# Kernel optimization log

Hardware: AMD Instinct MI355X
Metric: run time of the kernel (lower is better)

The kernel has to match this reference:

```python
import jax, jax.numpy as jnp
import numpy as np
import math

B, S, D, K = 8, 2048, 1024, 64
EPS = 1e-5

def _ln(x):
    m = jnp.mean(x, axis=-1, keepdims=True)
    v = jnp.mean((x - m) ** 2, axis=-1, keepdims=True)
    return (x - m) * jax.lax.rsqrt(v + EPS)

def setup_inputs() -> dict:
    key = jax.random.key(0)
    ks = jax.random.split(key, 14)
    s = 0.02
    return {
        "x":  jax.random.normal(ks[0], (B, S, D), dtype=jnp.float32),
        "Wk": jax.random.normal(ks[1], (D, K), dtype=jnp.float32) * s,
        "bk": jnp.zeros((K,), dtype=jnp.float32),
        "Wq": jax.random.normal(ks[2], (D, K), dtype=jnp.float32) * s,
        "bq": jnp.zeros((K,), dtype=jnp.float32),
        "Wv": jax.random.normal(ks[3], (D, D), dtype=jnp.float32) * s,
        "bv": jnp.zeros((D,), dtype=jnp.float32),
        "Wb": jax.random.normal(ks[4], (D, 1), dtype=jnp.float32) * s,
        "bb": jnp.zeros((1,), dtype=jnp.float32),
        "W1": jax.random.normal(ks[5], (D, D), dtype=jnp.float32) * s,
        "b1": jnp.zeros((D,), dtype=jnp.float32),
        "g1": jnp.ones((D,), dtype=jnp.float32),
        "be1": jnp.zeros((D,), dtype=jnp.float32),
    }

def reference(x, Wk, bk, Wq, bq, Wv, bv, Wb, bb, W1, b1, g1, be1):
    scale = 1.0 / math.sqrt(K)
    keys    = (jnp.einsum('bsd,dk->bsk', x, Wk) + bk) * scale   # [B,S,K]
    queries = jnp.einsum('bsd,dk->bsk', x, Wq) + bq             # [B,S,K]
    values  = jnp.einsum('bsd,de->bse', x, Wv) + bv             # [B,S,D]
    biases  = jnp.einsum('bsd,do->bso', x, Wb) + bb             # [B,S,1]
    # scores[b,i,j] = keys[b,i] . queries[b,j] + biases[b,i]
    scores = jax.nn.sigmoid(jnp.einsum('bik,bjk->bij', keys, queries) + biases)
    attention = jnp.einsum('bij,bjd->bid', scores, values)      # [B,S,D]
    res = _ln(x + attention) * g1 + be1
    feedforward = jax.nn.relu(jnp.einsum('bsd,de->bse', res, W1) + b1)
    return _ln(res + feedforward)
```

## Files before the change

kernel.cpp:

```cpp
#include <hip/hip_runtime.h>
#include <math.h>


typedef __bf16 bf16_t;
typedef __bf16 bf16x2_t __attribute__((ext_vector_type(2)));
typedef __bf16 bf16x4_t __attribute__((ext_vector_type(4)));
typedef __bf16 bf16x8_t __attribute__((ext_vector_type(8)));
typedef float  f32x4    __attribute__((ext_vector_type(4)));

#define DEV static __device__ __forceinline__

DEV void gll16(const void* g, void* l) {
  __builtin_amdgcn_global_load_lds(
      (const __attribute__((address_space(1))) void*)g,
      (__attribute__((address_space(3))) void*)l, 16, 0, 0);
}

template <int MODE, int MFAST>
__global__ __launch_bounds__(512, 2) void gemm256(
    const bf16_t* __restrict__ A, const bf16_t* __restrict__ B,
    bf16_t* __restrict__ C, int K, int lda, int ldb, int ldc,
    long sAb, long sBb, long sCb, const float* __restrict__ aux0) {
  const int gx = gridDim.x, gy = gridDim.y;
  const int gxy = gx * gy;
  const int nwg = gxy * (int)gridDim.z;
  const int orig = blockIdx.x + gx * blockIdx.y + gxy * blockIdx.z;
  const int lid = (orig & 7) * (nwg >> 3) + (orig >> 3);
  const int bz = lid / gxy;
  const int rem = lid - bz * gxy;
  const int bx = MFAST ? (rem / gy) : (rem % gx);
  const int by = MFAST ? (rem % gy) : (rem / gx);

  A += (long)bz * sAb;
  B += (long)bz * sBb;
  const int m0 = by * 256, n0 = bx * 256;

  __shared__ bf16_t As[2][2][256 * 32];
  __shared__ bf16_t Bs[2][2][256 * 32];

  const int tid = threadIdx.x;
  const int wid = tid >> 6, l = tid & 63;
  const int wr = wid >> 2, wc = wid & 3;
  const int lr = l & 15, lh = l >> 4;

  const int sRow = tid >> 2;
  const int sSl = (tid & 3) ^ ((tid >> 3) & 3);
  const bf16_t* Asrc = A + (long)(m0 + sRow) * lda + sSl * 8;
  const bf16_t* Bsrc = B + (long)(n0 + sRow) * ldb + sSl * 8;
  const long aStep = (long)128 * lda, bStep = (long)128 * ldb;

#define STAGE_A(b, h, kt) do { \
    const bf16_t* s_ = Asrc + (kt) * 64 + (h) * 32; \
    gll16(s_,         &As[b][h][tid * 8]); \
    gll16(s_ + aStep, &As[b][h][4096 + tid * 8]); } while (0)
#define STAGE_B(b, h, kt) do { \
    const bf16_t* s_ = Bsrc + (kt) * 64 + (h) * 32; \
    gll16(s_,         &Bs[b][h][tid * 8]); \
    gll16(s_ + bStep, &Bs[b][h][4096 + tid * 8]); } while (0)

  const int sw = (lh ^ ((lr >> 1) & 3)) * 8;
  const int aOff = (wr * 128 + lr) * 32 + sw;
  const int bOff = (wc * 64 + lr) * 32 + sw;

  f32x4 acc[8][4] = {};
  const int NT = K >> 6;

  STAGE_A(0, 0, 0); STAGE_B(0, 0, 0); STAGE_A(0, 1, 0); STAGE_B(0, 1, 0);
  asm volatile("s_waitcnt vmcnt(4)" ::: "memory");
  __builtin_amdgcn_s_barrier();

#define PHASE_SYNC() do { \
    __builtin_amdgcn_sched_barrier(0); \
    __builtin_amdgcn_s_barrier(); \
    asm volatile("s_waitcnt lgkmcnt(0)" ::: "memory"); \
    __builtin_amdgcn_sched_barrier(0); } while (0)
#define MFMA_LO() do { \
    __builtin_amdgcn_s_setprio(1); \
    _Pragma("unroll") for (int m = 0; m < 4; ++m) \
    _Pragma("unroll") for (int n = 0; n < 4; ++n) \
      acc[m][n] = __builtin_amdgcn_mfma_f32_16x16x32_bf16(aF[m], bF[n], acc[m][n], 0, 0, 0); \
    __builtin_amdgcn_s_setprio(0); } while (0)
#define MFMA_HI() do { \
    __builtin_amdgcn_s_setprio(1); \
    _Pragma("unroll") for (int m = 0; m < 4; ++m) \
    _Pragma("unroll") for (int n = 0; n < 4; ++n) \
      acc[m + 4][n] = __builtin_amdgcn_mfma_f32_16x16x32_bf16(aG[m], bF[n], acc[m + 4][n], 0, 0, 0); \
    __builtin_amdgcn_s_setprio(0); } while (0)

  for (int t = 0; t < NT; ++t) {
    const int p = t & 1, q = p ^ 1;
    const bool pf = (t + 1 < NT);
    bf16x8_t bF[4], aF[4], aG[4];

#pragma unroll
    for (int n = 0; n < 4; ++n) bF[n] = *(const bf16x8_t*)&Bs[p][0][bOff + n * 512];
#pragma unroll
    for (int m = 0; m < 4; ++m) aF[m] = *(const bf16x8_t*)&As[p][0][aOff + m * 512];
    if (pf) STAGE_A(q, 0, t + 1);
    PHASE_SYNC();
    MFMA_LO();

#pragma unroll
    for (int m = 0; m < 4; ++m) aG[m] = *(const bf16x8_t*)&As[p][0][aOff + (m + 4) * 512];
    if (pf) {
      STAGE_B(q, 0, t + 1);
      asm volatile("s_waitcnt vmcnt(4)" ::: "memory");
    } else {
      asm volatile("s_waitcnt vmcnt(0)" ::: "memory");
    }
    PHASE_SYNC();
    MFMA_HI();

#pragma unroll
    for (int n = 0; n < 4; ++n) bF[n] = *(const bf16x8_t*)&Bs[p][1][bOff + n * 512];
#pragma unroll
    for (int m = 0; m < 4; ++m) aF[m] = *(const bf16x8_t*)&As[p][1][aOff + m * 512];
    if (pf) STAGE_A(q, 1, t + 1);
    PHASE_SYNC();
    MFMA_LO();

#pragma unroll
    for (int m = 0; m < 4; ++m) aG[m] = *(const bf16x8_t*)&As[p][1][aOff + (m + 4) * 512];
    if (pf) {
      STAGE_B(q, 1, t + 1);
      asm volatile("s_waitcnt vmcnt(4)" ::: "memory");
    }
    PHASE_SYNC();
    MFMA_HI();
  }
#undef STAGE_A
#undef STAGE_B
#undef PHASE_SYNC
#undef MFMA_LO
#undef MFMA_HI

  bf16_t* Cb = C + (long)bz * sCb;
  const int rowb = m0 + wr * 128 + lh * 4;
  const int colb = n0 + wc * 64 + lr;
#pragma unroll
  for (int m = 0; m < 8; ++m)
#pragma unroll
    for (int n = 0; n < 4; ++n) {
      const f32x4 v = acc[m][n];
      const int cc = colb + n * 16;
#pragma unroll
      for (int r = 0; r < 4; ++r) {
        const int rr = rowb + m * 16 + r;
        const float val = v[r];
        if constexpr (MODE == 1) {
          Cb[(long)rr * ldc + cc] = (bf16_t)(val + aux0[rr]);
        } else if constexpr (MODE == 3) {
          Cb[(long)rr * ldc + cc] = (bf16_t)val;
        } else {
          Cb[(long)rr * ldc + cc] = (bf16_t)fmaxf(val + aux0[cc], 0.0f);
        }
      }
    }
}

template <int MODE, int MFAST>
__global__ __launch_bounds__(256) void gemm_bt(
    const bf16_t* __restrict__ A, const bf16_t* __restrict__ B,
    void* __restrict__ Cv, int M, int N, int K, int lda, int ldb, int ldc,
    long sAb, long sBb, long sCb,
    const float* __restrict__ aux0, const float* __restrict__ aux1, long sAux) {
  const int gx = gridDim.x, gy = gridDim.y;
  const int gxy = gx * gy;
  const int nwg = gxy * (int)gridDim.z;
  const int orig = blockIdx.x + gx * blockIdx.y + gxy * blockIdx.z;
  const int q = nwg >> 3, r8 = nwg & 7;
  const int xcd = orig & 7, seq = orig >> 3;
  const int lid = (xcd < r8 ? xcd * (q + 1) : r8 * (q + 1) + (xcd - r8) * q) + seq;
  const int bz = lid / gxy;
  const int rem = lid - bz * gxy;
  const int bx = MFAST ? (rem / gy) : (rem % gx);
  const int by = MFAST ? (rem % gy) : (rem / gx);

  A += (long)bz * sAb;
  B += (long)bz * sBb;
  const float* a0 = (MODE == 2) ? (aux0 + (long)bz * sAux) : aux0;

  const int m0 = by * 128;
  const int n0 = bx * 128;

  __shared__ bf16_t As[2][128 * 32];
  __shared__ bf16_t Bs[2][128 * 32];

  const int tid = threadIdx.x;
  const int w = tid >> 6, l = tid & 63;
  const int wr = w >> 1, wc = w & 1;
  const int lr = l & 15, lh = l >> 4;

  const int srow = l >> 2;
  const int scol = (((l & 3) ^ (srow & 3)) << 3);

  f32x4 acc[4][4] = {};

  auto stage = [&](int buf, int k0) {
#pragma unroll
    for (int half = 0; half < 2; ++half) {
      const int i = 2 * w + half;
      const int row = (i << 4) + srow;
      gll16(A + (long)(m0 + row) * lda + k0 + scol, &As[buf][i << 9]);
      gll16(B + (long)(n0 + row) * ldb + k0 + scol, &Bs[buf][i << 9]);
    }
  };

  stage(0, 0);
  __syncthreads();
  int cur = 0;
  const int sw = ((lh ^ (lr & 3)) << 3);

  for (int k0 = 0; k0 < K; k0 += 32) {
    if (k0 + 32 < K) stage(cur ^ 1, k0 + 32);

    bf16x8_t af[4], bfm[4];
#pragma unroll
    for (int m = 0; m < 4; ++m)
      af[m] = *(const bf16x8_t*)(&As[cur][(((wr << 6) + (m << 4) + lr) << 5) + sw]);
#pragma unroll
    for (int n = 0; n < 4; ++n)
      bfm[n] = *(const bf16x8_t*)(&Bs[cur][(((wc << 6) + (n << 4) + lr) << 5) + sw]);
#pragma unroll
    for (int m = 0; m < 4; ++m)
#pragma unroll
      for (int n = 0; n < 4; ++n)
        acc[m][n] = __builtin_amdgcn_mfma_f32_16x16x32_bf16(af[m], bfm[n], acc[m][n], 0, 0, 0);

    __syncthreads();
    cur ^= 1;
  }

  const int rowbase = m0 + (wr << 6) + (lh << 2);
  const int colbase = n0 + (wc << 6) + lr;
#pragma unroll
  for (int m = 0; m < 4; ++m) {
#pragma unroll
    for (int n = 0; n < 4; ++n) {
      const f32x4 v = acc[m][n];
      const int cc = colbase + (n << 4);
#pragma unroll
      for (int r = 0; r < 4; ++r) {
        const int rr = rowbase + (m << 4) + r;
        const float val = v[r];
        if constexpr (MODE == 0) {
          const float b = (cc < 64) ? aux0[cc] : aux1[cc - 64];
          const float s = (cc < 64) ? 0.125f : 1.0f;
          ((bf16_t*)Cv)[(long)rr * ldc + cc] = (bf16_t)((val + b) * s);
        } else {
          const float zz = val + a0[rr];
          const float e = __expf(-zz);
          const float sg = __builtin_amdgcn_rcpf(1.0f + e);
          ((bf16_t*)Cv)[(long)bz * sCb + (long)rr * ldc + cc] = (bf16_t)sg;
        }
      }
    }
  }
}

__global__ __launch_bounds__(256) void cast_bf16_kernel(
    const float* __restrict__ in, bf16_t* __restrict__ out, long n) {
  long i = ((long)blockIdx.x * 256 + threadIdx.x) * 4;
  const long step = (long)gridDim.x * 1024;
  for (; i < n; i += step) {
    const float4 v = *(const float4*)(in + i);
    bf16x4_t o;
    o[0] = (bf16_t)v.x; o[1] = (bf16_t)v.y; o[2] = (bf16_t)v.z; o[3] = (bf16_t)v.w;
    *(bf16x4_t*)(out + i) = o;
  }
}

__global__ __launch_bounds__(256) void transpose_cast_kernel(
    const float* __restrict__ in, bf16_t* __restrict__ out, int R, int C) {
  __shared__ float t[32][33];
  const int c0 = blockIdx.x * 32, r0 = blockIdx.y * 32;
  const int tx = threadIdx.x & 31, ty = threadIdx.x >> 5;
#pragma unroll
  for (int i = 0; i < 4; ++i) {
    const int rl = ty * 4 + i;
    t[rl][tx] = in[(long)(r0 + rl) * C + c0 + tx];
  }
  __syncthreads();
#pragma unroll
  for (int i = 0; i < 4; ++i) {
    const int rl = ty * 4 + i;
    out[(long)(c0 + rl) * R + r0 + tx] = (bf16_t)t[tx][rl];
  }
}

__global__ __launch_bounds__(256) void bias_kernel(
    const bf16_t* __restrict__ x, const float* __restrict__ Wb,
    const float* __restrict__ bb, float* __restrict__ biases) {
  const int r = blockIdx.x * 4 + (threadIdx.x >> 6);
  const int l = threadIdx.x & 63;
  const bf16_t* xr = x + (long)r * 1024;
  float s = 0.f;
#pragma unroll
  for (int i = 0; i < 8; ++i) {
    const bf16x2_t v = *(const bf16x2_t*)(xr + (l << 1) + (i << 7));
    const float2 wv = *(const float2*)(Wb + (l << 1) + (i << 7));
    s += (float)v[0] * wv.x + (float)v[1] * wv.y;
  }
#pragma unroll
  for (int off = 1; off < 64; off <<= 1) s += __shfl_xor(s, off);
  if (l == 0) biases[r] = s + bb[0];
}

DEV float2 block_sum2(float s, float ss) {
#pragma unroll
  for (int off = 1; off < 64; off <<= 1) {
    s += __shfl_xor(s, off);
    ss += __shfl_xor(ss, off);
  }
  __shared__ float bs[4], bss[4];
  const int w = threadIdx.x >> 6, l = threadIdx.x & 63;
  if (l == 0) { bs[w] = s; bss[w] = ss; }
  __syncthreads();
  s = bs[0] + bs[1] + bs[2] + bs[3];
  ss = bss[0] + bss[1] + bss[2] + bss[3];
  return make_float2(s, ss);
}

__global__ __launch_bounds__(256) void ln1_kernel(
    const bf16_t* __restrict__ x, const bf16_t* __restrict__ attn,
    const float* __restrict__ g, const float* __restrict__ be,
    bf16_t* __restrict__ res) {
  const long r = blockIdx.x;
  const int t = threadIdx.x;
  const bf16x4_t xv = *(const bf16x4_t*)(x + r * 1024 + t * 4);
  const bf16x4_t av = *(const bf16x4_t*)(attn + r * 1024 + t * 4);
  const float y0 = (float)xv[0] + (float)av[0], y1 = (float)xv[1] + (float)av[1];
  const float y2 = (float)xv[2] + (float)av[2], y3 = (float)xv[3] + (float)av[3];
  const float2 s2 = block_sum2(y0 + y1 + y2 + y3, y0 * y0 + y1 * y1 + y2 * y2 + y3 * y3);
  const float mean = s2.x * (1.0f / 1024.0f);
  const float var = s2.y * (1.0f / 1024.0f) - mean * mean;
  const float rs = rsqrtf(var + 1e-5f);
  const int c = t * 4;
  bf16x4_t o;
  o[0] = (bf16_t)((y0 - mean) * rs * g[c + 0] + be[c + 0]);
  o[1] = (bf16_t)((y1 - mean) * rs * g[c + 1] + be[c + 1]);
  o[2] = (bf16_t)((y2 - mean) * rs * g[c + 2] + be[c + 2]);
  o[3] = (bf16_t)((y3 - mean) * rs * g[c + 3] + be[c + 3]);
  *(bf16x4_t*)(res + r * 1024 + c) = o;
}

__global__ __launch_bounds__(256) void ln2_kernel(
    const bf16_t* __restrict__ res, const bf16_t* __restrict__ h,
    float* __restrict__ out) {
  const long r = blockIdx.x;
  const int t = threadIdx.x;
  const bf16x4_t rv = *(const bf16x4_t*)(res + r * 1024 + t * 4);
  const bf16x4_t hv = *(const bf16x4_t*)(h + r * 1024 + t * 4);
  const float y0 = (float)rv[0] + (float)hv[0], y1 = (float)rv[1] + (float)hv[1];
  const float y2 = (float)rv[2] + (float)hv[2], y3 = (float)rv[3] + (float)hv[3];
  const float2 s2 = block_sum2(y0 + y1 + y2 + y3, y0 * y0 + y1 * y1 + y2 * y2 + y3 * y3);
  const float mean = s2.x * (1.0f / 1024.0f);
  const float var = s2.y * (1.0f / 1024.0f) - mean * mean;
  const float rs = rsqrtf(var + 1e-5f);
  float4 o;
  o.x = (y0 - mean) * rs; o.y = (y1 - mean) * rs;
  o.z = (y2 - mean) * rs; o.w = (y3 - mean) * rs;
  ((float4*)(out + r * 1024))[t] = o;
}

extern "C" void kernel_launch(void* const* d_in, const int* in_sizes, int n_in,
                              void* d_out, int out_size, void* d_ws, size_t ws_size,
                              hipStream_t stream) {
  const float* x   = (const float*)d_in[0];
  const float* Wk  = (const float*)d_in[1];
  const float* bk  = (const float*)d_in[2];
  const float* Wq  = (const float*)d_in[3];
  const float* bq  = (const float*)d_in[4];
  const float* Wv  = (const float*)d_in[5];
  const float* bv  = (const float*)d_in[6];
  const float* Wb  = (const float*)d_in[7];
  const float* bb  = (const float*)d_in[8];
  const float* W1  = (const float*)d_in[9];
  const float* b1  = (const float*)d_in[10];
  const float* g1  = (const float*)d_in[11];
  const float* be1 = (const float*)d_in[12];
  float* out = (float*)d_out;

  char* ws = (char*)d_ws;
  bf16_t* x_bf    = (bf16_t*)(ws + 0);
  bf16_t* vt_bf   = (bf16_t*)(ws + 33554432);
  bf16_t* kq_bf   = (bf16_t*)(ws + 67108864);
  bf16_t* Wkqt    = (bf16_t*)(ws + 71303168);
  bf16_t* Wvt     = (bf16_t*)(ws + 71565312);
  bf16_t* W1t     = (bf16_t*)(ws + 73662464);
  float*  biases  = (float*) (ws + 75759616);
  bf16_t* scores  = (bf16_t*)(ws + 75825152);
  bf16_t* attn_bf = (bf16_t*)(ws + 142934016);
  bf16_t* res_bf  = (bf16_t*)(ws + 176488448);
  bf16_t* h_bf    = attn_bf;

  const long BS = 16384;

  cast_bf16_kernel<<<8192, 256, 0, stream>>>(x, x_bf, BS * 1024);
  transpose_cast_kernel<<<dim3(2, 32), 256, 0, stream>>>(Wk, Wkqt, 1024, 64);
  transpose_cast_kernel<<<dim3(2, 32), 256, 0, stream>>>(Wq, Wkqt + 64 * 1024, 1024, 64);
  transpose_cast_kernel<<<dim3(32, 32), 256, 0, stream>>>(Wv, Wvt, 1024, 1024);
  transpose_cast_kernel<<<dim3(32, 32), 256, 0, stream>>>(W1, W1t, 1024, 1024);
  bias_kernel<<<4096, 256, 0, stream>>>(x_bf, Wb, bb, biases);

  gemm_bt<0, 0><<<dim3(1, 128, 1), 256, 0, stream>>>(
      x_bf, Wkqt, kq_bf, 16384, 128, 1024, 1024, 1024, 128, 0, 0, 0, bk, bq, 0);

  gemm256<1, 1><<<dim3(64, 4, 1), 512, 0, stream>>>(
      Wvt, x_bf, vt_bf, 1024, 1024, 1024, 16384, 0, 0, 0, bv);

  gemm_bt<2, 0><<<dim3(16, 16, 8), 256, 0, stream>>>(
      kq_bf, kq_bf + 64, scores, 2048, 2048, 64, 128, 128, 2048,
      2048L * 128, 2048L * 128, 2048L * 2048, biases, nullptr, 2048);

  gemm256<3, 0><<<dim3(4, 8, 8), 512, 0, stream>>>(
      scores, vt_bf, attn_bf, 2048, 2048, 16384, 1024,
      2048L * 2048, 2048, 2048L * 1024, nullptr);

  ln1_kernel<<<16384, 256, 0, stream>>>(x_bf, attn_bf, g1, be1, res_bf);

  gemm256<4, 0><<<dim3(4, 64, 1), 512, 0, stream>>>(
      res_bf, W1t, h_bf, 1024, 1024, 1024, 1024, 0, 0, 0, b1);

  ln2_kernel<<<16384, 256, 0, stream>>>(res_bf, h_bf, out);
}
```

Before: 254.4 us.

## Stage GEMM epilogues through LDS for vector stores; fuse cast with bias

Both GEMM kernels now write their outputs through a swizzled shared-memory tile (reusing the staging buffers as one flat array) and then emit 16-byte coalesced global stores, instead of scattered 2-byte stores per accumulator element. The input cast and the bias dot product are fused into one kernel that reads x in fp32 once. This removes a launch and an extra pass over x_bf, and bias now uses fp32 x rather than bf16-rounded x. The vmcnt wait in the last phase is made unconditional, and the epilogue adds barriers and LDS traffic.

```diff
diff --git a/kernel.cpp b/kernel.cpp
--- a/kernel.cpp
+++ b/kernel.cpp
@@ -3,7 +3,6 @@
 
 
 typedef __bf16 bf16_t;
-typedef __bf16 bf16x2_t __attribute__((ext_vector_type(2)));
 typedef __bf16 bf16x4_t __attribute__((ext_vector_type(4)));
 typedef __bf16 bf16x8_t __attribute__((ext_vector_type(8)));
 typedef float  f32x4    __attribute__((ext_vector_type(4)));
@@ -35,8 +34,9 @@
   B += (long)bz * sBb;
   const int m0 = by * 256, n0 = bx * 256;
 
-  __shared__ bf16_t As[2][2][256 * 32];
-  __shared__ bf16_t Bs[2][2][256 * 32];
+  __shared__ bf16_t SM[65536];
+#define ASH(b, h) (&SM[(((b)*2 + (h)) << 13)])
+#define BSH(b, h) (&SM[32768 + (((b)*2 + (h)) << 13)])
 
   const int tid = threadIdx.x;
   const int wid = tid >> 6, l = tid & 63;
@@ -51,12 +51,12 @@
 
 #define STAGE_A(b, h, kt) do { \
     const bf16_t* s_ = Asrc + (kt) * 64 + (h) * 32; \
-    gll16(s_,         &As[b][h][tid * 8]); \
-    gll16(s_ + aStep, &As[b][h][4096 + tid * 8]); } while (0)
+    gll16(s_,         ASH(b, h) + tid * 8); \
+    gll16(s_ + aStep, ASH(b, h) + 4096 + tid * 8); } while (0)
 #define STAGE_B(b, h, kt) do { \
     const bf16_t* s_ = Bsrc + (kt) * 64 + (h) * 32; \
-    gll16(s_,         &Bs[b][h][tid * 8]); \
-    gll16(s_ + bStep, &Bs[b][h][4096 + tid * 8]); } while (0)
+    gll16(s_,         BSH(b, h) + tid * 8); \
+    gll16(s_ + bStep, BSH(b, h) + 4096 + tid * 8); } while (0)
 
   const int sw = (lh ^ ((lr >> 1) & 3)) * 8;
   const int aOff = (wr * 128 + lr) * 32 + sw;
@@ -93,15 +93,15 @@
     bf16x8_t bF[4], aF[4], aG[4];
 
 #pragma unroll
-    for (int n = 0; n < 4; ++n) bF[n] = *(const bf16x8_t*)&Bs[p][0][bOff + n * 512];
-#pragma unroll
-    for (int m = 0; m < 4; ++m) aF[m] = *(const bf16x8_t*)&As[p][0][aOff + m * 512];
+    for (int n = 0; n < 4; ++n) bF[n] = *(const bf16x8_t*)(BSH(p, 0) + bOff + n * 512);
+#pragma unroll
+    for (int m = 0; m < 4; ++m) aF[m] = *(const bf16x8_t*)(ASH(p, 0) + aOff + m * 512);
     if (pf) STAGE_A(q, 0, t + 1);
     PHASE_SYNC();
     MFMA_LO();
 
 #pragma unroll
-    for (int m = 0; m < 4; ++m) aG[m] = *(const bf16x8_t*)&As[p][0][aOff + (m + 4) * 512];
+    for (int m = 0; m < 4; ++m) aG[m] = *(const bf16x8_t*)(ASH(p, 0) + aOff + (m + 4) * 512);
     if (pf) {
       STAGE_B(q, 0, t + 1);
       asm volatile("s_waitcnt vmcnt(4)" ::: "memory");
@@ -112,19 +112,17 @@
     MFMA_HI();
 
 #pragma unroll
-    for (int n = 0; n < 4; ++n) bF[n] = *(const bf16x8_t*)&Bs[p][1][bOff + n * 512];
-#pragma unroll
-    for (int m = 0; m < 4; ++m) aF[m] = *(const bf16x8_t*)&As[p][1][aOff + m * 512];
+    for (int n = 0; n < 4; ++n) bF[n] = *(const bf16x8_t*)(BSH(p, 1) + bOff + n * 512);
+#pragma unroll
+    for (int m = 0; m < 4; ++m) aF[m] = *(const bf16x8_t*)(ASH(p, 1) + aOff + m * 512);
     if (pf) STAGE_A(q, 1, t + 1);
     PHASE_SYNC();
     MFMA_LO();
 
 #pragma unroll
-    for (int m = 0; m < 4; ++m) aG[m] = *(const bf16x8_t*)&As[p][1][aOff + (m + 4) * 512];
-    if (pf) {
-      STAGE_B(q, 1, t + 1);
-      asm volatile("s_waitcnt vmcnt(4)" ::: "memory");
-    }
+    for (int m = 0; m < 4; ++m) aG[m] = *(const bf16x8_t*)(ASH(p, 1) + aOff + (m + 4) * 512);
+    if (pf) STAGE_B(q, 1, t + 1);
+    asm volatile("s_waitcnt vmcnt(4)" ::: "memory");
     PHASE_SYNC();
     MFMA_HI();
   }
@@ -134,28 +132,38 @@
 #undef MFMA_LO
 #undef MFMA_HI
 
-  bf16_t* Cb = C + (long)bz * sCb;
-  const int rowb = m0 + wr * 128 + lh * 4;
-  const int colb = n0 + wc * 64 + lr;
-#pragma unroll
-  for (int m = 0; m < 8; ++m)
-#pragma unroll
-    for (int n = 0; n < 4; ++n) {
-      const f32x4 v = acc[m][n];
-      const int cc = colb + n * 16;
-#pragma unroll
-      for (int r = 0; r < 4; ++r) {
-        const int rr = rowb + m * 16 + r;
-        const float val = v[r];
-        if constexpr (MODE == 1) {
-          Cb[(long)rr * ldc + cc] = (bf16_t)(val + aux0[rr]);
-        } else if constexpr (MODE == 3) {
-          Cb[(long)rr * ldc + cc] = (bf16_t)val;
-        } else {
-          Cb[(long)rr * ldc + cc] = (bf16_t)fmaxf(val + aux0[cc], 0.0f);
+  __builtin_amdgcn_s_barrier();
+  {
+    const int rowb = wr * 128 + lh * 4;
+    const int colb = wc * 64 + lr;
+#pragma unroll
+    for (int m = 0; m < 8; ++m)
+#pragma unroll
+      for (int n = 0; n < 4; ++n) {
+        const f32x4 v = acc[m][n];
+        const int cl = colb + n * 16;
+#pragma unroll
+        for (int r = 0; r < 4; ++r) {
+          const int rl = rowb + m * 16 + r;
+          float val = v[r];
+          if constexpr (MODE == 1) val += aux0[m0 + rl];
+          else if constexpr (MODE == 4) val = fmaxf(val + aux0[n0 + cl], 0.0f);
+          SM[rl * 256 + (cl ^ (lh << 4))] = (bf16_t)val;
         }
       }
+    __builtin_amdgcn_s_barrier();
+    bf16_t* Cb = C + (long)bz * sCb;
+    const int chunk = tid & 31, rsub = tid >> 5;
+#pragma unroll
+    for (int pp = 0; pp < 16; ++pp) {
+      const int rl = pp * 16 + rsub;
+      const int sc = chunk ^ (((rl >> 2) & 3) << 1);
+      const bf16x8_t vv = *(const bf16x8_t*)&SM[rl * 256 + sc * 8];
+      *(bf16x8_t*)&Cb[(long)(m0 + rl) * ldc + n0 + chunk * 8] = vv;
     }
+  }
+#undef ASH
+#undef BSH
 }
 
 template <int MODE, int MFAST>
@@ -183,8 +191,9 @@
   const int m0 = by * 128;
   const int n0 = bx * 128;
 
-  __shared__ bf16_t As[2][128 * 32];
-  __shared__ bf16_t Bs[2][128 * 32];
+  __shared__ bf16_t SM[16384];
+#define ASH(b) (&SM[(b) << 12])
+#define BSH(b) (&SM[8192 + ((b) << 12)])
 
   const int tid = threadIdx.x;
   const int w = tid >> 6, l = tid & 63;
@@ -201,8 +210,8 @@
     for (int half = 0; half < 2; ++half) {
       const int i = 2 * w + half;
       const int row = (i << 4) + srow;
-      gll16(A + (long)(m0 + row) * lda + k0 + scol, &As[buf][i << 9]);
-      gll16(B + (long)(n0 + row) * ldb + k0 + scol, &Bs[buf][i << 9]);
+      gll16(A + (long)(m0 + row) * lda + k0 + scol, ASH(buf) + (i << 9));
+      gll16(B + (long)(n0 + row) * ldb + k0 + scol, BSH(buf) + (i << 9));
     }
   };
 
@@ -217,10 +226,10 @@
     bf16x8_t af[4], bfm[4];
 #pragma unroll
     for (int m = 0; m < 4; ++m)
-      af[m] = *(const bf16x8_t*)(&As[cur][(((wr << 6) + (m << 4) + lr) << 5) + sw]);
+      af[m] = *(const bf16x8_t*)(ASH(cur) + (((wr << 6) + (m << 4) + lr) << 5) + sw);
 #pragma unroll
     for (int n = 0; n < 4; ++n)
-      bfm[n] = *(const bf16x8_t*)(&Bs[cur][(((wc << 6) + (n << 4) + lr) << 5) + sw]);
+      bfm[n] = *(const bf16x8_t*)(BSH(cur) + (((wc << 6) + (n << 4) + lr) << 5) + sw);
 #pragma unroll
     for (int m = 0; m < 4; ++m)
 #pragma unroll
@@ -231,43 +240,67 @@
     cur ^= 1;
   }
 
-  const int rowbase = m0 + (wr << 6) + (lh << 2);
-  const int colbase = n0 + (wc << 6) + lr;
-#pragma unroll
-  for (int m = 0; m < 4; ++m) {
-#pragma unroll
-    for (int n = 0; n < 4; ++n) {
-      const f32x4 v = acc[m][n];
-      const int cc = colbase + (n << 4);
-#pragma unroll
-      for (int r = 0; r < 4; ++r) {
-        const int rr = rowbase + (m << 4) + r;
-        const float val = v[r];
-        if constexpr (MODE == 0) {
-          const float b = (cc < 64) ? aux0[cc] : aux1[cc - 64];
-          const float s = (cc < 64) ? 0.125f : 1.0f;
-          ((bf16_t*)Cv)[(long)rr * ldc + cc] = (bf16_t)((val + b) * s);
-        } else {
-          const float zz = val + a0[rr];
-          const float e = __expf(-zz);
-          const float sg = __builtin_amdgcn_rcpf(1.0f + e);
-          ((bf16_t*)Cv)[(long)bz * sCb + (long)rr * ldc + cc] = (bf16_t)sg;
+  {
+    const int rowb = (wr << 6) + (lh << 2);
+    const int colb = (wc << 6) + lr;
+#pragma unroll
+    for (int m = 0; m < 4; ++m)
+#pragma unroll
+      for (int n = 0; n < 4; ++n) {
+        const f32x4 v = acc[m][n];
+        const int cl = colb + (n << 4);
+#pragma unroll
+        for (int r = 0; r < 4; ++r) {
+          const int rl = rowb + (m << 4) + r;
+          float val = v[r];
+          if constexpr (MODE == 0) {
+            const int cc = n0 + cl;
+            const float b = (cc < 64) ? aux0[cc] : aux1[cc - 64];
+            val = (cc < 64) ? (val + b) * 0.125f : (val + b);
+          } else {
+            const float zz = val + a0[m0 + rl];
+            val = __builtin_amdgcn_rcpf(1.0f + __expf(-zz));
+          }
+          SM[rl * 128 + (cl ^ (lh << 4))] = (bf16_t)val;
         }
       }
+    __syncthreads();
+    bf16_t* Cb = (bf16_t*)Cv + (MODE == 2 ? (long)bz * sCb : 0L);
+    const int chunk = tid & 15, rsub = tid >> 4;
+#pragma unroll
+    for (int pp = 0; pp < 8; ++pp) {
+      const int rl = pp * 16 + rsub;
+      const int sc = chunk ^ (((rl >> 2) & 3) << 1);
+      const bf16x8_t vv = *(const bf16x8_t*)&SM[rl * 128 + sc * 8];
+      *(bf16x8_t*)&Cb[(long)(m0 + rl) * ldc + n0 + chunk * 8] = vv;
     }
   }
-}
-
-__global__ __launch_bounds__(256) void cast_bf16_kernel(
-    const float* __restrict__ in, bf16_t* __restrict__ out, long n) {
-  long i = ((long)blockIdx.x * 256 + threadIdx.x) * 4;
-  const long step = (long)gridDim.x * 1024;
-  for (; i < n; i += step) {
-    const float4 v = *(const float4*)(in + i);
+#undef ASH
+#undef BSH
+}
+
+__global__ __launch_bounds__(256) void cast_bias_kernel(
+    const float* __restrict__ x, const float* __restrict__ Wb,
+    const float* __restrict__ bb, bf16_t* __restrict__ x_bf,
+    float* __restrict__ biases) {
+  const int r = blockIdx.x * 4 + (threadIdx.x >> 6);
+  const int l = threadIdx.x & 63;
+  const float* xr = x + (long)r * 1024;
+  bf16_t* orow = x_bf + (long)r * 1024;
+  float s = 0.f;
+#pragma unroll
+  for (int i = 0; i < 4; ++i) {
+    const int off = l * 4 + i * 256;
+    const float4 v = *(const float4*)(xr + off);
+    const float4 w = *(const float4*)(Wb + off);
+    s += v.x * w.x + v.y * w.y + v.z * w.z + v.w * w.w;
     bf16x4_t o;
     o[0] = (bf16_t)v.x; o[1] = (bf16_t)v.y; o[2] = (bf16_t)v.z; o[3] = (bf16_t)v.w;
-    *(bf16x4_t*)(out + i) = o;
-  }
+    *(bf16x4_t*)(orow + off) = o;
+  }
+#pragma unroll
+  for (int off = 1; off < 64; off <<= 1) s += __shfl_xor(s, off);
+  if (l == 0) biases[r] = s + bb[0];
 }
 
 __global__ __launch_bounds__(256) void transpose_cast_kernel(
@@ -286,24 +319,6 @@
     const int rl = ty * 4 + i;
     out[(long)(c0 + rl) * R + r0 + tx] = (bf16_t)t[tx][rl];
   }
-}
-
-__global__ __launch_bounds__(256) void bias_kernel(
-    const bf16_t* __restrict__ x, const float* __restrict__ Wb,
-    const float* __restrict__ bb, float* __restrict__ biases) {
-  const int r = blockIdx.x * 4 + (threadIdx.x >> 6);
-  const int l = threadIdx.x & 63;
-  const bf16_t* xr = x + (long)r * 1024;
-  float s = 0.f;
-#pragma unroll
-  for (int i = 0; i < 8; ++i) {
-    const bf16x2_t v = *(const bf16x2_t*)(xr + (l << 1) + (i << 7));
-    const float2 wv = *(const float2*)(Wb + (l << 1) + (i << 7));
-    s += (float)v[0] * wv.x + (float)v[1] * wv.y;
-  }
-#pragma unroll
-  for (int off = 1; off < 64; off <<= 1) s += __shfl_xor(s, off);
-  if (l == 0) biases[r] = s + bb[0];
 }
 
 DEV float2 block_sum2(float s, float ss) {
@@ -394,14 +409,11 @@
   bf16_t* res_bf  = (bf16_t*)(ws + 176488448);
   bf16_t* h_bf    = attn_bf;
 
-  const long BS = 16384;
-
-  cast_bf16_kernel<<<8192, 256, 0, stream>>>(x, x_bf, BS * 1024);
+  cast_bias_kernel<<<4096, 256, 0, stream>>>(x, Wb, bb, x_bf, biases);
   transpose_cast_kernel<<<dim3(2, 32), 256, 0, stream>>>(Wk, Wkqt, 1024, 64);
   transpose_cast_kernel<<<dim3(2, 32), 256, 0, stream>>>(Wq, Wkqt + 64 * 1024, 1024, 64);
   transpose_cast_kernel<<<dim3(32, 32), 256, 0, stream>>>(Wv, Wvt, 1024, 1024);
   transpose_cast_kernel<<<dim3(32, 32), 256, 0, stream>>>(W1, W1t, 1024, 1024);
-  bias_kernel<<<4096, 256, 0, stream>>>(x_bf, Wb, bb, biases);
 
   gemm_bt<0, 0><<<dim3(1, 128, 1), 256, 0, stream>>>(
       x_bf, Wkqt, kq_bf, 16384, 128, 1024, 1024, 1024, 128, 0, 0, 0, bk, bq, 0);
```

New measurement: 252.4 us. Within noise of the previous version (-0.8%).
